# Kernel tuning notes

Measured on AMD Instinct MI355X. Metric: run time of the kernel, lower is better.

The kernel has to match this reference:

```python
import jax, jax.numpy as jnp
import numpy as np

N_NODES = 50000
N_HEDGES = 10000
N_MEMB = 800000
IN_SIZE = 256
HEADS = 4
OUT_SIZE = 64


def setup_inputs() -> dict:
    key = jax.random.key(0)
    k1, k2, k3, k4, k5 = jax.random.split(key, 5)
    x = jax.random.normal(k1, (N_NODES, IN_SIZE), dtype=jnp.float32)
    # Linear weight stored as [in, out*heads] so projection is x @ W (same math as torch Linear)
    W = jax.random.normal(k2, (IN_SIZE, OUT_SIZE * HEADS), dtype=jnp.float32) * (1.0 / np.sqrt(IN_SIZE))
    att_e = jax.random.normal(k3, (1, HEADS, OUT_SIZE), dtype=jnp.float32) * 0.1
    node_idx = jax.random.randint(k4, (N_MEMB,), 0, N_NODES, dtype=jnp.int64)
    hedge_idx = jax.random.randint(k5, (N_MEMB,), 0, N_HEDGES, dtype=jnp.int64)
    return {"x": x, "W": W, "att_e": att_e, "node_idx": node_idx,
            "hedge_idx": hedge_idx, "num_hyperedges": N_HEDGES}


def reference(x, W, att_e, node_idx, hedge_idx, num_hyperedges):
    # Dropout is treated as eval-mode identity.
    N = x.shape[0]
    H, D = att_e.shape[1], att_e.shape[2]
    xp = (x @ W).reshape(N, H, D)                                   # [N,H,D]
    # Stage 1: mean-aggregate node features into hyperedges (belongs-to)
    ones = jnp.ones(node_idx.shape[0], dtype=x.dtype)
    deg = jax.ops.segment_sum(ones, hedge_idx, num_segments=num_hyperedges)  # [E]
    he = jax.ops.segment_sum(xp[node_idx], hedge_idx, num_segments=num_hyperedges)
    he = he / jnp.maximum(deg, 1.0)[:, None, None]                  # [E,H,D]
    # Attention logit per hyperedge
    alpha_e = jax.nn.leaky_relu(jnp.sum(he * att_e, axis=-1), 0.2)  # [E,H]
    # Stage 2: edge_softmax over 'contains' edges grouped by destination node
    ae = alpha_e[hedge_idx]                                         # [M,H]
    mx = jax.ops.segment_max(ae, node_idx, num_segments=N)          # [N,H]
    ex = jnp.exp(ae - mx[node_idx])
    den = jax.ops.segment_sum(ex, node_idx, num_segments=N)         # [N,H]
    a = ex / den[node_idx]                                          # [M,H]
    # Attention-weighted scatter-sum of hyperedge features to nodes
    out = jax.ops.segment_sum(he[hedge_idx] * a[:, :, None], node_idx, num_segments=N)  # [N,H,D]
    return out.reshape(N, H * D)
```

## Files before the change

kernel.cpp:

```cpp
#include <hip/hip_runtime.h>
#include <hip/hip_fp16.h>
#include <math.h>

#define N_NODES  50000
#define N_HEDGES 10000
#define N_MEMB   800000
#define KIN      256
#define CH       256
#define HEADS    4
#define HCAP     160
#define NCAP     48

#define NCHUNK      125
#define CHUNK4      1600
#define XCVT_F4     3200000
#define XCVT_BLOCKS 1563
#define WCVT_BLOCKS 8
#define HED_W       2500
#define NOD_W       12500

typedef _Float16 half2v __attribute__((ext_vector_type(2)));

__device__ inline float2 h2f(unsigned u) {
    __half2 h = __builtin_bit_cast(__half2, u);
    return __half22float2(h);
}
__device__ inline unsigned f2h(float a, float b) {
    return __builtin_bit_cast(unsigned, __floats2half2_rn(a, b));
}
__device__ inline float4 u2tof4(uint2 u) {
    float2 lo = h2f(u.x), hi = h2f(u.y);
    return make_float4(lo.x, lo.y, hi.x, hi.y);
}
__device__ inline void acc4(float4& a, float4 f) {
    a.x += f.x; a.y += f.y; a.z += f.z; a.w += f.w;
}
__device__ inline void fmaU4(float4& A, float4& B, float w, uint4 g) {
    float2 f0 = h2f(g.x), f1 = h2f(g.y), f2 = h2f(g.z), f3 = h2f(g.w);
    A.x += w * f0.x; A.y += w * f0.y; A.z += w * f1.x; A.w += w * f1.y;
    B.x += w * f2.x; B.y += w * f2.y; B.z += w * f3.x; B.w += w * f3.y;
}
__device__ inline float fdot2w(half2v a, half2v b, float c) {
#if __has_builtin(__builtin_amdgcn_fdot2)
    return __builtin_amdgcn_fdot2(a, b, c, false);
#else
    return c + (float)a.x * (float)b.x + (float)a.y * (float)b.y;
#endif
}

__global__ __launch_bounds__(1024)
void k_hist_cvt(const int4* __restrict__ ni4, const int4* __restrict__ hi4,
                unsigned char* __restrict__ htab, unsigned char* __restrict__ ntab,
                const float4* __restrict__ x4, uint2* __restrict__ x16,
                const float* __restrict__ Wf, unsigned* __restrict__ Wp) {
    __shared__ unsigned sh[HED_W + NOD_W];
    int bid = blockIdx.x, tid = threadIdx.x;
    if (bid < NCHUNK) {
        int chunk = bid;
        for (int i = tid; i < HED_W + NOD_W; i += 1024) sh[i] = 0;
        __syncthreads();
        int base4 = chunk * CHUNK4;
        for (int i = tid; i < CHUNK4; i += 1024) {
            int4 e = hi4[base4 + i]; int4 n = ni4[base4 + i];
            #pragma unroll
            for (int k = 0; k < 4; k++) {
                int ev = (&e.x)[k], nv = (&n.x)[k];
                atomicAdd(&sh[ev >> 2], 1u << ((ev & 3) * 8));
                atomicAdd(&sh[HED_W + (nv >> 2)], 1u << ((nv & 3) * 8));
            }
        }
        __syncthreads();
        unsigned* hd = (unsigned*)(htab + (size_t)chunk * N_HEDGES);
        for (int i = tid; i < HED_W; i += 1024) hd[i] = sh[i];
        unsigned* nd = (unsigned*)(ntab + (size_t)chunk * N_NODES);
        for (int i = tid; i < NOD_W; i += 1024) nd[i] = sh[HED_W + i];
    } else if (bid < NCHUNK + XCVT_BLOCKS) {
        int i0 = (bid - NCHUNK) * 2048 + tid;
        #pragma unroll
        for (int r = 0; r < 2; r++) {
            int idx = i0 + r * 1024;
            if (idx < XCVT_F4) {
                float4 v = x4[idx];
                uint2 u; u.x = f2h(v.x, v.y); u.y = f2h(v.z, v.w);
                x16[idx] = u;
            }
        }
    } else {
        int tg = (bid - NCHUNK - XCVT_BLOCKS) * 1024 + tid;
        #pragma unroll
        for (int r = 0; r < 4; r++) {
            int wI = tg + r * 8192;
            int k2 = wI >> 8, c = wI & 255;
            Wp[wI] = f2h(Wf[(size_t)(2 * k2) * CH + c], Wf[(size_t)(2 * k2 + 1) * CH + c]);
        }
    }
}

__global__ __launch_bounds__(1024)
void k_scan(unsigned char* __restrict__ htab, unsigned char* __restrict__ ntab,
            int* __restrict__ hdeg, int* __restrict__ ndeg) {
    int b = blockIdx.x * 1024 + threadIdx.x;
    if (b < N_HEDGES) {
        int run = 0;
        for (int c = 0; c < NCHUNK; c++) {
            size_t idx = (size_t)c * N_HEDGES + b;
            int v = htab[idx];
            htab[idx] = (unsigned char)run;
            run += v;
        }
        hdeg[b] = run;
    } else if (b < N_HEDGES + N_NODES) {
        int nb = b - N_HEDGES;
        int run = 0;
        for (int c = 0; c < NCHUNK; c++) {
            size_t idx = (size_t)c * N_NODES + nb;
            int v = ntab[idx];
            ntab[idx] = (unsigned char)run;
            run += v;
        }
        ndeg[nb] = run;
    }
}

__global__ __launch_bounds__(1024)
void k_place(const int4* __restrict__ ni4, const int4* __restrict__ hi4,
             const unsigned char* __restrict__ htab, const unsigned char* __restrict__ ntab,
             int* __restrict__ hmem, int* __restrict__ nhedge) {
    __shared__ unsigned sh[HED_W + NOD_W];
    int bid = blockIdx.x, tid = threadIdx.x;
    int chunk = bid;
    for (int i = tid; i < HED_W + NOD_W; i += 1024) sh[i] = 0;
    __syncthreads();
    int base4 = chunk * CHUNK4;
    const unsigned char* hoff = htab + (size_t)chunk * N_HEDGES;
    const unsigned char* noff = ntab + (size_t)chunk * N_NODES;
    for (int i = tid; i < CHUNK4; i += 1024) {
        int4 e = hi4[base4 + i]; int4 n = ni4[base4 + i];
        #pragma unroll
        for (int k = 0; k < 4; k++) {
            int ev = (&e.x)[k], nv = (&n.x)[k];
            unsigned oldh = atomicAdd(&sh[ev >> 2], 1u << ((ev & 3) * 8));
            int rh = (int)((oldh >> ((ev & 3) * 8)) & 0xffu);
            int posh = (int)hoff[ev] + rh;
            if (posh < HCAP) hmem[(size_t)ev * HCAP + posh] = nv;
            unsigned oldn = atomicAdd(&sh[HED_W + (nv >> 2)], 1u << ((nv & 3) * 8));
            int rn = (int)((oldn >> ((nv & 3) * 8)) & 0xffu);
            int posn = (int)noff[nv] + rn;
            if (posn < NCAP) nhedge[(size_t)nv * NCAP + posn] = ev;
        }
    }
}

__global__ __launch_bounds__(256, 6)
void k_stage1(const int* __restrict__ hdeg, const int* __restrict__ hmem,
              const uint2* __restrict__ x16, const unsigned* __restrict__ Wp,
              const float* __restrict__ att, __half* __restrict__ he,
              float* __restrict__ alpha) {
    __shared__ int sidx[4][HCAP];
    __shared__ unsigned hxT[KIN / 2][4];
    int tid = threadIdx.x;
    int w = tid >> 6, lt = tid & 63;
    int e0 = blockIdx.x * 4;
    int e = e0 + w;
    int deg = hdeg[e];
    int degC = min(deg, HCAP);
    const int* ml = hmem + (size_t)e * HCAP;
    for (int j = lt; j < degC; j += 64) sidx[w][j] = ml[j];
    __syncthreads();
    float4 ac0 = {0,0,0,0}, ac1 = {0,0,0,0}, ac2 = {0,0,0,0}, ac3 = {0,0,0,0};
    for (int j = 0; j < degC; j += 16) {
        uint2 g[16];
        #pragma unroll
        for (int i = 0; i < 16; i++) {
            int jj = j + i; jj = jj < degC ? jj : degC - 1;
            g[i] = x16[(size_t)sidx[w][jj] * 64 + lt];
        }
        #pragma unroll
        for (int i = 0; i < 16; i++) {
            if (j + i < degC) {
                if ((i & 3) == 0) acc4(ac0, u2tof4(g[i]));
                else if ((i & 3) == 1) acc4(ac1, u2tof4(g[i]));
                else if ((i & 3) == 2) acc4(ac2, u2tof4(g[i]));
                else acc4(ac3, u2tof4(g[i]));
            }
        }
    }
    float sx = (ac0.x + ac1.x) + (ac2.x + ac3.x);
    float sy = (ac0.y + ac1.y) + (ac2.y + ac3.y);
    float sz = (ac0.z + ac1.z) + (ac2.z + ac3.z);
    float sw = (ac0.w + ac1.w) + (ac2.w + ac3.w);
    float inv = deg > 0 ? 1.0f / (float)deg : 0.0f;
    hxT[2 * lt][w]     = f2h(sx * inv, sy * inv);
    hxT[2 * lt + 1][w] = f2h(sz * inv, sw * inv);
    __syncthreads();
    int c = tid;
    float a0 = 0.f, a1 = 0.f, a2 = 0.f, a3 = 0.f;
    for (int k2 = 0; k2 < KIN / 2; k2++) {
        unsigned wv = Wp[(size_t)k2 * CH + c];
        half2v wh = __builtin_bit_cast(half2v, wv);
        uint4 hq = *(const uint4*)&hxT[k2][0];
        a0 = fdot2w(__builtin_bit_cast(half2v, hq.x), wh, a0);
        a1 = fdot2w(__builtin_bit_cast(half2v, hq.y), wh, a1);
        a2 = fdot2w(__builtin_bit_cast(half2v, hq.z), wh, a2);
        a3 = fdot2w(__builtin_bit_cast(half2v, hq.w), wh, a3);
    }
    he[(size_t)(e0 + 0) * CH + c] = __float2half_rn(a0);
    he[(size_t)(e0 + 1) * CH + c] = __float2half_rn(a1);
    he[(size_t)(e0 + 2) * CH + c] = __float2half_rn(a2);
    he[(size_t)(e0 + 3) * CH + c] = __float2half_rn(a3);
    float av = att[c];
    float p0 = a0 * av, p1 = a1 * av, p2 = a2 * av, p3 = a3 * av;
    #pragma unroll
    for (int d = 32; d >= 1; d >>= 1) {
        p0 += __shfl_xor(p0, d, 64); p1 += __shfl_xor(p1, d, 64);
        p2 += __shfl_xor(p2, d, 64); p3 += __shfl_xor(p3, d, 64);
    }
    if (lt == 0) {
        alpha[(e0 + 0) * HEADS + w] = p0 > 0.f ? p0 : 0.2f * p0;
        alpha[(e0 + 1) * HEADS + w] = p1 > 0.f ? p1 : 0.2f * p1;
        alpha[(e0 + 2) * HEADS + w] = p2 > 0.f ? p2 : 0.2f * p2;
        alpha[(e0 + 3) * HEADS + w] = p3 > 0.f ? p3 : 0.2f * p3;
    }
}

__global__ __launch_bounds__(256, 8)
void k_stage2(const uint4* __restrict__ heu4, const float4* __restrict__ alpha4,
              const int* __restrict__ ndeg, const int* __restrict__ nhedge,
              float4* __restrict__ out) {
    __shared__ int   nh[4][NCAP];
    __shared__ float wl[4][4][NCAP];
    int tid = threadIdx.x;
    int w = tid >> 6, L = tid & 63;
    int half = L >> 5, q = L & 31;
    int n = blockIdx.x * 4 + w;
    int deg = min(ndeg[n], NCAP);
    const int* nl = nhedge + (size_t)n * NCAP;
    if (L < deg) nh[w][L] = nl[L];
    __syncthreads();
    float4 mx = make_float4(-INFINITY, -INFINITY, -INFINITY, -INFINITY);
    float4 w4 = make_float4(0.f, 0.f, 0.f, 0.f);
    float4 aj = mx;
    if (L < deg) { aj = alpha4[nh[w][L]]; mx = aj; }
    #pragma unroll
    for (int d = 32; d >= 1; d >>= 1) {
        mx.x = fmaxf(mx.x, __shfl_xor(mx.x, d, 64));
        mx.y = fmaxf(mx.y, __shfl_xor(mx.y, d, 64));
        mx.z = fmaxf(mx.z, __shfl_xor(mx.z, d, 64));
        mx.w = fmaxf(mx.w, __shfl_xor(mx.w, d, 64));
    }
    if (L < deg) {
        w4.x = __expf(aj.x - mx.x); w4.y = __expf(aj.y - mx.y);
        w4.z = __expf(aj.z - mx.z); w4.w = __expf(aj.w - mx.w);
        wl[w][0][L] = w4.x; wl[w][1][L] = w4.y;
        wl[w][2][L] = w4.z; wl[w][3][L] = w4.w;
    }
    float4 dn = w4;
    #pragma unroll
    for (int d = 32; d >= 1; d >>= 1) {
        dn.x += __shfl_xor(dn.x, d, 64);
        dn.y += __shfl_xor(dn.y, d, 64);
        dn.z += __shfl_xor(dn.z, d, 64);
        dn.w += __shfl_xor(dn.w, d, 64);
    }
    __syncthreads();
    int h = q >> 3;
    float den = h < 2 ? (h == 0 ? dn.x : dn.y) : (h == 2 ? dn.z : dn.w);
    float4 A = make_float4(0.f, 0.f, 0.f, 0.f);
    float4 B = make_float4(0.f, 0.f, 0.f, 0.f);
    if (deg > 0) {
        for (int j = 0; j < deg; j += 8) {
            uint4 g[4]; float wgt[4];
            #pragma unroll
            for (int i = 0; i < 4; i++) {
                int jj = j + 2 * i + half;
                int jc = jj < deg ? jj : deg - 1;
                wgt[i] = jj < deg ? wl[w][h][jc] : 0.f;
                g[i] = heu4[(size_t)nh[w][jc] * 32 + q];
            }
            #pragma unroll
            for (int i = 0; i < 4; i++) fmaU4(A, B, wgt[i], g[i]);
        }
    }
    A.x += __shfl_xor(A.x, 32, 64); A.y += __shfl_xor(A.y, 32, 64);
    A.z += __shfl_xor(A.z, 32, 64); A.w += __shfl_xor(A.w, 32, 64);
    B.x += __shfl_xor(B.x, 32, 64); B.y += __shfl_xor(B.y, 32, 64);
    B.z += __shfl_xor(B.z, 32, 64); B.w += __shfl_xor(B.w, 32, 64);
    if (half == 0) {
        if (deg > 0) {
            float inv = 1.0f / den;
            A.x *= inv; A.y *= inv; A.z *= inv; A.w *= inv;
            B.x *= inv; B.y *= inv; B.z *= inv; B.w *= inv;
        }
        out[(size_t)n * 64 + 2 * q]     = A;
        out[(size_t)n * 64 + 2 * q + 1] = B;
    }
}

extern "C" void kernel_launch(void* const* d_in, const int* in_sizes, int n_in,
                              void* d_out, int out_size, void* d_ws, size_t ws_size,
                              hipStream_t stream) {
    const float* x        = (const float*)d_in[0];
    const float* W        = (const float*)d_in[1];
    const float* att      = (const float*)d_in[2];
    const int*   node_idx = (const int*)d_in[3];
    const int*   hedge_idx= (const int*)d_in[4];
    float4* out4 = (float4*)d_out;

    char* ws = (char*)d_ws;
    size_t o = 0;
    auto alloc = [&](size_t b) { size_t r = o; o += (b + 255) & ~(size_t)255; return r; };
    float* alpha = (float*)(ws + alloc(sizeof(float) * (size_t)N_HEDGES * HEADS));
    unsigned* Wp = (unsigned*)(ws + alloc(sizeof(unsigned) * (KIN / 2) * CH));
    int*   hdeg  = (int*)(ws + alloc(sizeof(int) * N_HEDGES));
    int*   ndeg  = (int*)(ws + alloc(sizeof(int) * N_NODES));
    int*   hmem  = (int*)(ws + alloc(sizeof(int) * (size_t)N_HEDGES * HCAP));
    __half* he   = (__half*)(ws + alloc(sizeof(__half) * (size_t)N_HEDGES * CH));
    int*   nhedge = (int*)(ws + alloc(sizeof(int) * (size_t)N_NODES * NCAP));
    unsigned char* htab = (unsigned char*)(ws + alloc((size_t)NCHUNK * N_HEDGES));
    unsigned char* ntab = (unsigned char*)(ws + alloc((size_t)NCHUNK * N_NODES));
    if (o > ws_size) return;
    uint2* x16 = (uint2*)d_out;

    k_hist_cvt<<<NCHUNK + XCVT_BLOCKS + WCVT_BLOCKS, 1024, 0, stream>>>(
        (const int4*)node_idx, (const int4*)hedge_idx, htab, ntab,
        (const float4*)x, x16, W, Wp);
    k_scan<<<(N_HEDGES + N_NODES + 1023) / 1024, 1024, 0, stream>>>(htab, ntab, hdeg, ndeg);
    k_place<<<NCHUNK, 1024, 0, stream>>>(
        (const int4*)node_idx, (const int4*)hedge_idx, htab, ntab, hmem, nhedge);
    k_stage1<<<N_HEDGES / 4, 256, 0, stream>>>(hdeg, hmem, x16, Wp, att, he, alpha);
    k_stage2<<<N_NODES / 4, 256, 0, stream>>>((const uint4*)he, (const float4*)alpha,
                                              ndeg, nhedge, out4);
}
```

Measured before the change: 169.5 us.

## Project all nodes with MFMA GEMM before aggregation, fuse scan into GEMM launch

Instead of averaging raw fp16 x rows per hyperedge and then projecting the 10k hyperedge means with fdot2, the projection is now done first on all 50k nodes with an MFMA 16x16x32 fp16 GEMM that writes fp16 xp. Stage 1 then averages the projected rows and computes the attention logit with a per-head shuffle reduction. The separate x-conversion pass goes away and the degree scan shares a launch with the GEMM. The trade is about 5x more projection FLOPs (50k rows instead of 10k) in exchange for tensor-core throughput and one fewer launch and conversion pass.

```diff
diff --git a/kernel.cpp b/kernel.cpp
--- a/kernel.cpp
+++ b/kernel.cpp
@@ -13,13 +13,14 @@
 
 #define NCHUNK      125
 #define CHUNK4      1600
-#define XCVT_F4     3200000
-#define XCVT_BLOCKS 1563
-#define WCVT_BLOCKS 8
 #define HED_W       2500
 #define NOD_W       12500
-
-typedef _Float16 half2v __attribute__((ext_vector_type(2)));
+#define WT_BLOCKS   4
+#define GEMM_BLOCKS 782
+#define SCAN_BLOCKS 118
+
+typedef _Float16 v8h __attribute__((ext_vector_type(8)));
+typedef float v4f __attribute__((ext_vector_type(4)));
 
 __device__ inline float2 h2f(unsigned u) {
     __half2 h = __builtin_bit_cast(__half2, u);
@@ -40,19 +41,11 @@
     A.x += w * f0.x; A.y += w * f0.y; A.z += w * f1.x; A.w += w * f1.y;
     B.x += w * f2.x; B.y += w * f2.y; B.z += w * f3.x; B.w += w * f3.y;
 }
-__device__ inline float fdot2w(half2v a, half2v b, float c) {
-#if __has_builtin(__builtin_amdgcn_fdot2)
-    return __builtin_amdgcn_fdot2(a, b, c, false);
-#else
-    return c + (float)a.x * (float)b.x + (float)a.y * (float)b.y;
-#endif
-}
 
 __global__ __launch_bounds__(1024)
-void k_hist_cvt(const int4* __restrict__ ni4, const int4* __restrict__ hi4,
-                unsigned char* __restrict__ htab, unsigned char* __restrict__ ntab,
-                const float4* __restrict__ x4, uint2* __restrict__ x16,
-                const float* __restrict__ Wf, unsigned* __restrict__ Wp) {
+void k_hist_wt(const int4* __restrict__ ni4, const int4* __restrict__ hi4,
+               unsigned char* __restrict__ htab, unsigned char* __restrict__ ntab,
+               const float* __restrict__ Wf, _Float16* __restrict__ WT) {
     __shared__ unsigned sh[HED_W + NOD_W];
     int bid = blockIdx.x, tid = threadIdx.x;
     if (bid < NCHUNK) {
@@ -74,51 +67,97 @@
         for (int i = tid; i < HED_W; i += 1024) hd[i] = sh[i];
         unsigned* nd = (unsigned*)(ntab + (size_t)chunk * N_NODES);
         for (int i = tid; i < NOD_W; i += 1024) nd[i] = sh[HED_W + i];
-    } else if (bid < NCHUNK + XCVT_BLOCKS) {
-        int i0 = (bid - NCHUNK) * 2048 + tid;
-        #pragma unroll
-        for (int r = 0; r < 2; r++) {
-            int idx = i0 + r * 1024;
-            if (idx < XCVT_F4) {
-                float4 v = x4[idx];
-                uint2 u; u.x = f2h(v.x, v.y); u.y = f2h(v.z, v.w);
-                x16[idx] = u;
-            }
-        }
     } else {
-        int tg = (bid - NCHUNK - XCVT_BLOCKS) * 1024 + tid;
-        #pragma unroll
-        for (int r = 0; r < 4; r++) {
-            int wI = tg + r * 8192;
-            int k2 = wI >> 8, c = wI & 255;
-            Wp[wI] = f2h(Wf[(size_t)(2 * k2) * CH + c], Wf[(size_t)(2 * k2 + 1) * CH + c]);
-        }
-    }
-}
-
-__global__ __launch_bounds__(1024)
-void k_scan(unsigned char* __restrict__ htab, unsigned char* __restrict__ ntab,
-            int* __restrict__ hdeg, int* __restrict__ ndeg) {
-    int b = blockIdx.x * 1024 + threadIdx.x;
-    if (b < N_HEDGES) {
-        int run = 0;
-        for (int c = 0; c < NCHUNK; c++) {
-            size_t idx = (size_t)c * N_HEDGES + b;
-            int v = htab[idx];
-            htab[idx] = (unsigned char)run;
-            run += v;
-        }
-        hdeg[b] = run;
-    } else if (b < N_HEDGES + N_NODES) {
-        int nb = b - N_HEDGES;
-        int run = 0;
-        for (int c = 0; c < NCHUNK; c++) {
-            size_t idx = (size_t)c * N_NODES + nb;
-            int v = ntab[idx];
-            ntab[idx] = (unsigned char)run;
-            run += v;
-        }
-        ndeg[nb] = run;
+        int tg = (bid - NCHUNK) * 1024 + tid;
+        #pragma unroll
+        for (int i = 0; i < 16; i++) {
+            int idx = tg + i * 4096;
+            int k = idx >> 8, n = idx & 255;
+            WT[(size_t)n * KIN + k] = (_Float16)Wf[(size_t)k * CH + n];
+        }
+    }
+}
+
+__global__ __launch_bounds__(512)
+void k_gemm_scan(const float4* __restrict__ x4, const _Float16* __restrict__ WT,
+                 __half* __restrict__ xp,
+                 unsigned char* __restrict__ htab, unsigned char* __restrict__ ntab,
+                 int* __restrict__ hdeg, int* __restrict__ ndeg) {
+    __shared__ __align__(16) _Float16 As[64][264];
+    __shared__ __align__(16) _Float16 Bs[256][40];
+    int bid = blockIdx.x, tid = threadIdx.x;
+    if (bid < GEMM_BLOCKS) {
+        int m0 = bid * 64;
+        for (int i = tid; i < 4096; i += 512) {
+            int row = i >> 6, k4 = i & 63;
+            int gr = m0 + row; if (gr >= N_NODES) gr = N_NODES - 1;
+            float4 v = x4[(size_t)gr * 64 + k4];
+            uint2 u; u.x = f2h(v.x, v.y); u.y = f2h(v.z, v.w);
+            *(uint2*)&As[row][k4 * 4] = u;
+        }
+        int w = tid >> 6, l = tid & 63;
+        int mg = w & 3, nh = w >> 2;
+        int lr = l & 15, lk = l >> 4;
+        v4f acc[8];
+        #pragma unroll
+        for (int nt = 0; nt < 8; nt++) acc[nt] = (v4f){0.f, 0.f, 0.f, 0.f};
+#if __has_builtin(__builtin_amdgcn_mfma_f32_16x16x32_f16)
+        for (int ks = 0; ks < 8; ks++) {
+            int k0 = ks * 32;
+            __syncthreads();
+            for (int i = tid; i < 1024; i += 512) {
+                int n = i >> 2, q = i & 3;
+                *(uint4*)&Bs[n][q * 8] = *(const uint4*)&WT[(size_t)n * KIN + k0 + q * 8];
+            }
+            __syncthreads();
+            v8h a = *(const v8h*)&As[mg * 16 + lr][k0 + lk * 8];
+            #pragma unroll
+            for (int nt = 0; nt < 8; nt++) {
+                v8h b = *(const v8h*)&Bs[(nh * 8 + nt) * 16 + lr][lk * 8];
+                acc[nt] = __builtin_amdgcn_mfma_f32_16x16x32_f16(a, b, acc[nt], 0, 0, 0);
+            }
+        }
+        #pragma unroll
+        for (int nt = 0; nt < 8; nt++) {
+            int n = (nh * 8 + nt) * 16 + lr;
+            #pragma unroll
+            for (int r = 0; r < 4; r++) {
+                int row = m0 + mg * 16 + lk * 4 + r;
+                if (row < N_NODES) xp[(size_t)row * CH + n] = __float2half_rn(acc[nt][r]);
+            }
+        }
+#else
+        __syncthreads();
+        for (int i = tid; i < 64 * 256; i += 512) {
+            int row = i >> 8, n = i & 255;
+            float s = 0.f;
+            for (int k = 0; k < KIN; k++) s += (float)As[row][k] * (float)WT[(size_t)n * KIN + k];
+            int gr = m0 + row;
+            if (gr < N_NODES) xp[(size_t)gr * CH + n] = __float2half_rn(s);
+        }
+#endif
+    } else {
+        int b = (bid - GEMM_BLOCKS) * 512 + tid;
+        if (b < N_HEDGES) {
+            int run = 0;
+            for (int c = 0; c < NCHUNK; c++) {
+                size_t idx = (size_t)c * N_HEDGES + b;
+                int v = htab[idx];
+                htab[idx] = (unsigned char)run;
+                run += v;
+            }
+            hdeg[b] = run;
+        } else if (b < N_HEDGES + N_NODES) {
+            int nb = b - N_HEDGES;
+            int run = 0;
+            for (int c = 0; c < NCHUNK; c++) {
+                size_t idx = (size_t)c * N_NODES + nb;
+                int v = ntab[idx];
+                ntab[idx] = (unsigned char)run;
+                run += v;
+            }
+            ndeg[nb] = run;
+        }
     }
 }
 
@@ -151,17 +190,14 @@
     }
 }
 
-__global__ __launch_bounds__(256, 6)
+__global__ __launch_bounds__(256, 8)
 void k_stage1(const int* __restrict__ hdeg, const int* __restrict__ hmem,
-              const uint2* __restrict__ x16, const unsigned* __restrict__ Wp,
-              const float* __restrict__ att, __half* __restrict__ he,
-              float* __restrict__ alpha) {
+              const uint2* __restrict__ xp2, const float4* __restrict__ att4,
+              uint2* __restrict__ he2, float* __restrict__ alpha) {
     __shared__ int sidx[4][HCAP];
-    __shared__ unsigned hxT[KIN / 2][4];
     int tid = threadIdx.x;
     int w = tid >> 6, lt = tid & 63;
-    int e0 = blockIdx.x * 4;
-    int e = e0 + w;
+    int e = blockIdx.x * 4 + w;
     int deg = hdeg[e];
     int degC = min(deg, HCAP);
     const int* ml = hmem + (size_t)e * HCAP;
@@ -173,7 +209,7 @@
         #pragma unroll
         for (int i = 0; i < 16; i++) {
             int jj = j + i; jj = jj < degC ? jj : degC - 1;
-            g[i] = x16[(size_t)sidx[w][jj] * 64 + lt];
+            g[i] = xp2[(size_t)sidx[w][jj] * 64 + lt];
         }
         #pragma unroll
         for (int i = 0; i < 16; i++) {
@@ -190,36 +226,16 @@
     float sz = (ac0.z + ac1.z) + (ac2.z + ac3.z);
     float sw = (ac0.w + ac1.w) + (ac2.w + ac3.w);
     float inv = deg > 0 ? 1.0f / (float)deg : 0.0f;
-    hxT[2 * lt][w]     = f2h(sx * inv, sy * inv);
-    hxT[2 * lt + 1][w] = f2h(sz * inv, sw * inv);
-    __syncthreads();
-    int c = tid;
-    float a0 = 0.f, a1 = 0.f, a2 = 0.f, a3 = 0.f;
-    for (int k2 = 0; k2 < KIN / 2; k2++) {
-        unsigned wv = Wp[(size_t)k2 * CH + c];
-        half2v wh = __builtin_bit_cast(half2v, wv);
-        uint4 hq = *(const uint4*)&hxT[k2][0];
-        a0 = fdot2w(__builtin_bit_cast(half2v, hq.x), wh, a0);
-        a1 = fdot2w(__builtin_bit_cast(half2v, hq.y), wh, a1);
-        a2 = fdot2w(__builtin_bit_cast(half2v, hq.z), wh, a2);
-        a3 = fdot2w(__builtin_bit_cast(half2v, hq.w), wh, a3);
-    }
-    he[(size_t)(e0 + 0) * CH + c] = __float2half_rn(a0);
-    he[(size_t)(e0 + 1) * CH + c] = __float2half_rn(a1);
-    he[(size_t)(e0 + 2) * CH + c] = __float2half_rn(a2);
-    he[(size_t)(e0 + 3) * CH + c] = __float2half_rn(a3);
-    float av = att[c];
-    float p0 = a0 * av, p1 = a1 * av, p2 = a2 * av, p3 = a3 * av;
-    #pragma unroll
-    for (int d = 32; d >= 1; d >>= 1) {
-        p0 += __shfl_xor(p0, d, 64); p1 += __shfl_xor(p1, d, 64);
-        p2 += __shfl_xor(p2, d, 64); p3 += __shfl_xor(p3, d, 64);
-    }
-    if (lt == 0) {
-        alpha[(e0 + 0) * HEADS + w] = p0 > 0.f ? p0 : 0.2f * p0;
-        alpha[(e0 + 1) * HEADS + w] = p1 > 0.f ? p1 : 0.2f * p1;
-        alpha[(e0 + 2) * HEADS + w] = p2 > 0.f ? p2 : 0.2f * p2;
-        alpha[(e0 + 3) * HEADS + w] = p3 > 0.f ? p3 : 0.2f * p3;
+    float m0 = sx * inv, m1 = sy * inv, m2 = sz * inv, m3 = sw * inv;
+    uint2 o; o.x = f2h(m0, m1); o.y = f2h(m2, m3);
+    he2[(size_t)e * 64 + lt] = o;
+    float4 a4 = att4[lt];
+    float p = m0 * a4.x + m1 * a4.y + m2 * a4.z + m3 * a4.w;
+    p += __shfl_xor(p, 1, 64); p += __shfl_xor(p, 2, 64);
+    p += __shfl_xor(p, 4, 64); p += __shfl_xor(p, 8, 64);
+    if ((lt & 15) == 0) {
+        int h = lt >> 4;
+        alpha[e * HEADS + h] = p > 0.f ? p : 0.2f * p;
     }
 }
 
@@ -310,7 +326,7 @@
     size_t o = 0;
     auto alloc = [&](size_t b) { size_t r = o; o += (b + 255) & ~(size_t)255; return r; };
     float* alpha = (float*)(ws + alloc(sizeof(float) * (size_t)N_HEDGES * HEADS));
-    unsigned* Wp = (unsigned*)(ws + alloc(sizeof(unsigned) * (KIN / 2) * CH));
+    _Float16* WT = (_Float16*)(ws + alloc(sizeof(_Float16) * (size_t)KIN * CH));
     int*   hdeg  = (int*)(ws + alloc(sizeof(int) * N_HEDGES));
     int*   ndeg  = (int*)(ws + alloc(sizeof(int) * N_NODES));
     int*   hmem  = (int*)(ws + alloc(sizeof(int) * (size_t)N_HEDGES * HCAP));
@@ -319,15 +335,16 @@
     unsigned char* htab = (unsigned char*)(ws + alloc((size_t)NCHUNK * N_HEDGES));
     unsigned char* ntab = (unsigned char*)(ws + alloc((size_t)NCHUNK * N_NODES));
     if (o > ws_size) return;
-    uint2* x16 = (uint2*)d_out;
-
-    k_hist_cvt<<<NCHUNK + XCVT_BLOCKS + WCVT_BLOCKS, 1024, 0, stream>>>(
-        (const int4*)node_idx, (const int4*)hedge_idx, htab, ntab,
-        (const float4*)x, x16, W, Wp);
-    k_scan<<<(N_HEDGES + N_NODES + 1023) / 1024, 1024, 0, stream>>>(htab, ntab, hdeg, ndeg);
+    __half* xp = (__half*)d_out;
+
+    k_hist_wt<<<NCHUNK + WT_BLOCKS, 1024, 0, stream>>>(
+        (const int4*)node_idx, (const int4*)hedge_idx, htab, ntab, W, WT);
+    k_gemm_scan<<<GEMM_BLOCKS + SCAN_BLOCKS, 512, 0, stream>>>(
+        (const float4*)x, WT, xp, htab, ntab, hdeg, ndeg);
     k_place<<<NCHUNK, 1024, 0, stream>>>(
         (const int4*)node_idx, (const int4*)hedge_idx, htab, ntab, hmem, nhedge);
-    k_stage1<<<N_HEDGES / 4, 256, 0, stream>>>(hdeg, hmem, x16, Wp, att, he, alpha);
+    k_stage1<<<N_HEDGES / 4, 256, 0, stream>>>(hdeg, hmem, (const uint2*)xp,
+                                               (const float4*)att, (uint2*)he, alpha);
     k_stage2<<<N_NODES / 4, 256, 0, stream>>>((const uint4*)he, (const float4*)alpha,
                                               ndeg, nhedge, out4);
 }
```

Measured after the change: 178.9 us. 5.6% more time.
